# Optimization experiments

Hardware: AMD Instinct MI355X
Metric: run time of the kernel (lower is better)

The kernel has to match this reference:

```python
import jax, jax.numpy as jnp
import numpy as np

B, C, L, H, K, STRIDE = 8, 512, 2048, 8, 3, 1
D = C // H                       # head dim = 64
LQ = (L - K) // STRIDE + 1       # 'valid' conv output length = 2046
LN_EPS = 1e-5


def setup_inputs() -> dict:
    key = jax.random.key(0)
    ks = jax.random.split(key, 6)
    std = np.sqrt(2.0 / (C + C // H))  # init: sqrt(2 / sum(param.shape[:2]))
    inp = {
        "input": jax.random.normal(ks[0], (B, C, L), dtype=jnp.float32),
        "init_weight": jax.random.normal(ks[1], (B, C, LQ), dtype=jnp.float32),
        "q_w": jax.random.normal(ks[2], (C, C // H, K), dtype=jnp.float32) * std,
        "k_w": jax.random.normal(ks[3], (C, C // H, K), dtype=jnp.float32) * std,
        "v_w": jax.random.normal(ks[4], (C, C // H, K), dtype=jnp.float32) * std,
        "gamma": jnp.ones((C,), dtype=jnp.float32),
        "beta": jnp.zeros((C,), dtype=jnp.float32),
        # causal-style additive mask (1 above diagonal -> attention -= 1e9*mask)
        "mask": jnp.triu(jnp.ones((LQ, LQ), dtype=jnp.float32), k=1),
    }
    return inp


def _gconv(x, w):
    # x: [B, C, L], w: [C_out, C_in/groups, K] (torch OIH layout)
    return jax.lax.conv_general_dilated(
        x, w, window_strides=(STRIDE,), padding="VALID",
        dimension_numbers=("NCH", "OIH", "NCH"), feature_group_count=H)


def reference(input, init_weight, q_w, k_w, v_w, gamma, beta, mask):
    # grouped-conv QKV projections: [B, C, LQ]
    q = _gconv(input, q_w).reshape(B, H, D, LQ)
    k = _gconv(input, k_w).reshape(B, H, D, LQ)
    v = _gconv(input, v_w).reshape(B, H, D, LQ)

    # scores: q^T k per head; NOTE: faithful scale is 1/sqrt(multihead_num)
    att = jnp.einsum("bhdq,bhdk->bhqk", q, k)
    att = att / jnp.sqrt(jnp.asarray(H, att.dtype))
    att = att - 1e9 * mask  # broadcast [LQ, LQ] over [B, H, LQ, LQ]
    att = jax.nn.softmax(att, axis=-1)
    # dropout with p=0.0 is the identity (drop_rate=0.0)

    o = jnp.einsum("bhqk,bhdk->bhqd", att, v)          # [B, H, LQ, D]
    o = o.transpose(0, 2, 1, 3).reshape(B, LQ, C)       # merge heads (head-major channels)

    feat = o + init_weight.transpose(0, 2, 1)           # residual, [B, LQ, C]
    mu = jnp.mean(feat, axis=-1, keepdims=True)
    var = jnp.var(feat, axis=-1, keepdims=True)
    feat = (feat - mu) / jnp.sqrt(var + LN_EPS) * gamma + beta
    return feat  # [B, LQ, C]
```

## Files before the change

### kernel.cpp

```cpp
#include <hip/hip_runtime.h>

#define LQN 2046
#define LL  2048
#define CC  512
#define DD  64

typedef float  f32x4 __attribute__((ext_vector_type(4)));
typedef float  f32x2 __attribute__((ext_vector_type(2)));
typedef __bf16 b16x8 __attribute__((ext_vector_type(8)));
typedef unsigned int u32x4 __attribute__((ext_vector_type(4)));
typedef unsigned int u32x2 __attribute__((ext_vector_type(2)));

static __device__ __forceinline__ unsigned short f2bf(float f) {
  union { float f; unsigned u; } v; v.f = f;
  return (unsigned short)((v.u + 0x7fffu + ((v.u >> 16) & 1u)) >> 16);
}

static __device__ __forceinline__ unsigned cvtpk(float lo, float hi) {
  unsigned r;
  asm("v_cvt_pk_bf16_f32 %0, %1, %2" : "=v"(r) : "v"(lo), "v"(hi));
  return r;
}

static __device__ __forceinline__ f32x4 mfma16(b16x8 a, b16x8 b, f32x4 c) {
  return __builtin_amdgcn_mfma_f32_16x16x32_bf16(a, b, c, 0, 0, 0);
}

static __device__ __forceinline__ void glds16(const unsigned short* g, unsigned short* l) {
  __builtin_amdgcn_global_load_lds(
      (const __attribute__((address_space(1))) unsigned int*)(g),
      (__attribute__((address_space(3))) unsigned int*)(l),
      16, 0, 0);
}

__global__ __launch_bounds__(256) void conv_qkv_kernel(
    const float* __restrict__ in, const float* __restrict__ qw,
    const float* __restrict__ kw, const float* __restrict__ vw,
    unsigned short* __restrict__ qo, unsigned short* __restrict__ ko,
    unsigned short* __restrict__ vo)
{
  __shared__ __align__(16) unsigned short inT[130 * 72];
  __shared__ __align__(16) unsigned short buf[128 * 72];

  const int tile = blockIdx.x, g = blockIdx.y, b = blockIdx.z;
  const int t0 = tile * 128;
  const int tid = threadIdx.x;
  const int lane = tid & 63;
  const int wv = tid >> 6;
  const int r0 = lane & 15, qh = lane >> 4;

  {
    const int ci = tid & 63, ch = tid >> 6;
    const float* src = in + ((size_t)(b * CC + g * 64 + ci)) * LL;
    #pragma unroll
    for (int i = 0; i < 8; ++i) {
      int t = ch * 32 + i * 4;
      f32x4 d = *(const f32x4*)(src + t0 + t);
      inT[(t + 0) * 72 + ci] = f2bf(d.x);
      inT[(t + 1) * 72 + ci] = f2bf(d.y);
      inT[(t + 2) * 72 + ci] = f2bf(d.z);
      inT[(t + 3) * 72 + ci] = f2bf(d.w);
    }
    if (ch == 0) {
      #pragma unroll
      for (int e = 0; e < 2; ++e) {
        int t = 128 + e;
        int tg = t0 + t; if (tg > LL - 1) tg = LL - 1;
        inT[t * 72 + ci] = f2bf(src[tg]);
      }
    }
  }
  __syncthreads();

  const float* wptr[3] = {qw, kw, vw};
  const f32x4 zero4 = {0.f, 0.f, 0.f, 0.f};

  for (int p = 0; p < 3; ++p) {
    b16x8 aW[6];
    {
      const float* wb = wptr[p] + (size_t)(g * 64 + wv * 16 + r0) * 192;
      #pragma unroll
      for (int kc = 0; kc < 6; ++kc) {
        const int ktap = kc >> 1;
        const int cib = (kc & 1) * 32 + qh * 8;
        union { b16x8 v; unsigned short u[8]; } fr;
        #pragma unroll
        for (int j = 0; j < 8; ++j)
          fr.u[j] = f2bf(wb[(cib + j) * 3 + ktap]);
        aW[kc] = fr.v;
      }
    }
    f32x4 acc[8];
    #pragma unroll
    for (int nt = 0; nt < 8; ++nt) acc[nt] = zero4;
    #pragma unroll
    for (int kc = 0; kc < 6; ++kc) {
      const int radd = kc >> 1;
      const int colh = (kc & 1) * 32 + qh * 8;
      #pragma unroll
      for (int nt = 0; nt < 8; ++nt) {
        const int trow = nt * 16 + r0 + radd;
        b16x8 bI = *(const b16x8*)&inT[trow * 72 + colh];
        acc[nt] = mfma16(aW[kc], bI, acc[nt]);
      }
    }
    __syncthreads();
    if (p < 2) {
      const float qscl = (p == 0) ? 0.51006979f : 1.0f;
      #pragma unroll
      for (int nt = 0; nt < 8; ++nt) {
        const int t = nt * 16 + r0;
        #pragma unroll
        for (int r = 0; r < 4; ++r)
          buf[t * 72 + wv * 16 + qh * 4 + r] = f2bf(acc[nt][r] * qscl);
      }
      __syncthreads();
      unsigned short* dst = (p == 0 ? qo : ko) +
          ((size_t)(b * 8 + g) * LQN + t0) * DD;
      #pragma unroll
      for (int it = 0; it < 4; ++it) {
        const int id = it * 256 + tid;
        const int t = id >> 3, c8 = id & 7;
        if (t0 + t < LQN)
          *(u32x4*)(dst + t * DD + c8 * 8) = *(const u32x4*)&buf[t * 72 + c8 * 8];
      }
    } else {
      #pragma unroll
      for (int nt = 0; nt < 8; ++nt) {
        const int t = nt * 16 + r0;
        #pragma unroll
        for (int r = 0; r < 4; ++r)
          buf[(wv * 16 + qh * 4 + r) * 136 + t] = f2bf(acc[nt][r]);
      }
      __syncthreads();
      unsigned short* dst = vo + ((size_t)(b * CC + g * 64)) * LL + t0;
      #pragma unroll
      for (int it = 0; it < 4; ++it) {
        const int id = it * 256 + tid;
        const int row = id >> 4, c16 = id & 15;
        *(u32x4*)(dst + (size_t)row * LL + c16 * 8) =
            *(const u32x4*)&buf[row * 136 + c16 * 8];
      }
    }
    __syncthreads();
  }
}

static __device__ __forceinline__ void attn_tile(
    const unsigned short* __restrict__ Kl, const unsigned short* __restrict__ Vl,
    unsigned short* __restrict__ Pl,
    bool diag, int wv, int r0, int qh,
    b16x8 aQ0, b16x8 aQ1,
    f32x4 (&o)[4], float& mrun, float& lrun)
{
  f32x4 s[4];
  __builtin_amdgcn_s_setprio(1);
  #pragma unroll
  for (int nt = 0; nt < 4; ++nt) {
    const int krow = nt * 16 + r0;
    const unsigned short* kr = Kl + krow * 64;
    const int sw = krow & 7;
    b16x8 k0 = *(const b16x8*)(kr + ((qh ^ sw) * 8));
    b16x8 k1 = *(const b16x8*)(kr + (((4 + qh) ^ sw) * 8));
    f32x4 acc = {0.f, 0.f, 0.f, 0.f};
    acc = mfma16(k0, aQ0, acc);
    s[nt] = mfma16(k1, aQ1, acc);
  }
  __builtin_amdgcn_s_setprio(0);
  if (diag) {
    const int rowl = wv * 16 + r0;
    #pragma unroll
    for (int nt = 0; nt < 4; ++nt) {
      #pragma unroll
      for (int rr = 0; rr < 4; ++rr)
        if (nt * 16 + qh * 4 + rr > rowl) s[nt][rr] = -1e30f;
    }
  }
  f32x4 m01, m23;
  #pragma unroll
  for (int rr = 0; rr < 4; ++rr) {
    m01[rr] = fmaxf(s[0][rr], s[1][rr]);
    m23[rr] = fmaxf(s[2][rr], s[3][rr]);
  }
  #pragma unroll
  for (int rr = 0; rr < 4; ++rr) m01[rr] = fmaxf(m01[rr], m23[rr]);
  float mt = fmaxf(fmaxf(m01[0], m01[1]), fmaxf(m01[2], m01[3]));
  mt = fmaxf(mt, __shfl_xor(mt, 16));
  mt = fmaxf(mt, __shfl_xor(mt, 32));
  const float mn = fmaxf(mrun, mt);
  const float corr = __builtin_amdgcn_exp2f(mrun - mn);
  mrun = mn;
  #pragma unroll
  for (int nt = 0; nt < 4; ++nt)
    #pragma unroll
    for (int rr = 0; rr < 4; ++rr)
      s[nt][rr] = __builtin_amdgcn_exp2f(s[nt][rr] - mn);
  f32x4 t01, t23;
  #pragma unroll
  for (int rr = 0; rr < 4; ++rr) {
    t01[rr] = s[0][rr] + s[1][rr];
    t23[rr] = s[2][rr] + s[3][rr];
  }
  #pragma unroll
  for (int rr = 0; rr < 4; ++rr) t01[rr] += t23[rr];
  float sum = (t01[0] + t01[1]) + (t01[2] + t01[3]);
  sum += __shfl_xor(sum, 16);
  sum += __shfl_xor(sum, 32);
  lrun = lrun * corr + sum;
  const int xr = r0 & 7;
  unsigned short* pw = Pl + r0 * 64 + (qh & 1) * 4;
  #pragma unroll
  for (int nt = 0; nt < 4; ++nt) {
    u32x2 w;
    w.x = cvtpk(s[nt][0], s[nt][1]);
    w.y = cvtpk(s[nt][2], s[nt][3]);
    *(u32x2*)(pw + (((nt * 2 + (qh >> 1)) ^ xr) * 8)) = w;
  }
  #pragma unroll
  for (int rr = 0; rr < 4; ++rr) {
    const float cq = __shfl(corr, qh * 4 + rr);
    o[0][rr] *= cq; o[1][rr] *= cq; o[2][rr] *= cq; o[3][rr] *= cq;
  }
  __builtin_amdgcn_s_setprio(1);
  #pragma unroll
  for (int kc = 0; kc < 2; ++kc) {
    b16x8 aP = *(const b16x8*)(Pl + r0 * 64 + (((kc * 4 + qh) ^ xr) * 8));
    #pragma unroll
    for (int dt = 0; dt < 4; ++dt) {
      const int vrow = dt * 16 + r0;
      b16x8 bv = *(const b16x8*)(Vl + vrow * 64 + (((kc * 4 + qh) ^ (vrow & 7)) * 8));
      o[dt] = mfma16(aP, bv, o[dt]);
    }
  }
  __builtin_amdgcn_s_setprio(0);
}

static __device__ __forceinline__ void issue_tile(
    const unsigned short*& kSrc, const unsigned short*& vSrc,
    unsigned short* kDst, unsigned short* vDst)
{
  glds16(kSrc,          kDst);
  glds16(kSrc + 8 * DD, kDst + 512);
  glds16(vSrc,          vDst);
  glds16(vSrc + 8 * LL, vDst + 512);
  kSrc += 64 * DD;
  vSrc += 64;
}

static __device__ __forceinline__ void attn_epilogue(
    unsigned short* smem, const float* __restrict__ initw,
    float* __restrict__ out, int b, int h, int qt,
    int tid, int wv, int r0, int qh,
    f32x4 (&o)[4], float lrun)
{
  __syncthreads();
  float* initL = (float*)smem;
  const int cc = tid >> 2, qgrp = (tid & 3) * 16;
  const float* src = initw + (size_t)(b * CC + h * 64 + cc) * LQN;
  #pragma unroll
  for (int u = 0; u < 8; ++u) {
    int col = qt * 64 + qgrp + u * 2;
    if (col > LQN - 2) col = LQN - 2;
    f32x2 d = *(const f32x2*)(src + col);
    initL[cc * 65 + qgrp + u * 2]     = d.x;
    initL[cc * 65 + qgrp + u * 2 + 1] = d.y;
  }
  __syncthreads();
  #pragma unroll
  for (int r = 0; r < 4; ++r) {
    const float lq = __shfl(lrun, qh * 4 + r);
    const int ql = wv * 16 + qh * 4 + r;
    const int qgl = qt * 64 + ql;
    if (qgl >= LQN) continue;
    const float invl = 1.0f / lq;
    float* dst = out + ((size_t)(b * LQN + qgl)) * CC + h * 64;
    #pragma unroll
    for (int dt = 0; dt < 4; ++dt)
      dst[dt * 16 + r0] = o[dt][r] * invl + initL[(dt * 16 + r0) * 65 + ql];
  }
}

__global__ __launch_bounds__(256) void attn_kernel(
    const unsigned short* __restrict__ qg, const unsigned short* __restrict__ kg,
    const unsigned short* __restrict__ vg, const float* __restrict__ initw,
    float* __restrict__ out)
{
  __shared__ __align__(16) unsigned short KV[2][8192];
  __shared__ __align__(16) unsigned short Pb[4][1024];

  const int pi = blockIdx.x;
  const int hi = 31 - pi, lo = pi;
  const int bh = blockIdx.y;
  const int b = bh >> 3, h = bh & 7;
  const int tid = threadIdx.x, lane = tid & 63, wv = tid >> 6;
  const int r0 = lane & 15, qh = lane >> 4;

  const size_t kqbase = (size_t)bh * LQN * DD;
  const size_t vbase  = ((size_t)(b * CC + h * 64)) * LL;

  const int l8 = lane >> 3, c8s = lane & 7;
  const int csw = c8s ^ l8;
  const unsigned short* kSrc = kg + kqbase + (size_t)(wv * 16 + l8) * DD + csw * 8;
  const unsigned short* vSrc = vg + vbase  + (size_t)(wv * 16 + l8) * LL + csw * 8;

  b16x8 aQ0h, aQ1h, aQ0l, aQ1l;
  {
    int qrow = hi * 64 + wv * 16 + r0; if (qrow > LQN - 1) qrow = LQN - 1;
    const unsigned short* qp = qg + kqbase + (size_t)qrow * DD;
    aQ0h = *(const b16x8*)(qp + qh * 8);
    aQ1h = *(const b16x8*)(qp + 32 + qh * 8);
    qrow = lo * 64 + wv * 16 + r0;
    qp = qg + kqbase + (size_t)qrow * DD;
    aQ0l = *(const b16x8*)(qp + qh * 8);
    aQ1l = *(const b16x8*)(qp + 32 + qh * 8);
  }

  const f32x4 zero4 = {0.f, 0.f, 0.f, 0.f};
  f32x4 oh[4], ol[4];
  float mh = -1e30f, ml = -1e30f, lh = 0.f, llr = 0.f;
  #pragma unroll
  for (int dt = 0; dt < 4; ++dt) { oh[dt] = zero4; ol[dt] = zero4; }

  int bi = 0;
  issue_tile(kSrc, vSrc, &KV[0][wv * 1024], &KV[0][4096 + wv * 1024]);
  for (int kt = 0; kt <= hi; ++kt) {
    __syncthreads();
    if (kt < hi)
      issue_tile(kSrc, vSrc, &KV[bi ^ 1][wv * 1024], &KV[bi ^ 1][4096 + wv * 1024]);
    attn_tile(&KV[bi][0], &KV[bi][4096], Pb[wv], kt == hi, wv, r0, qh,
              aQ0h, aQ1h, oh, mh, lh);
    if (kt <= lo)
      attn_tile(&KV[bi][0], &KV[bi][4096], Pb[wv], kt == lo, wv, r0, qh,
                aQ0l, aQ1l, ol, ml, llr);
    bi ^= 1;
  }

  attn_epilogue(&KV[0][0], initw, out, b, h, hi, tid, wv, r0, qh, oh, lh);
  attn_epilogue(&KV[0][0], initw, out, b, h, lo, tid, wv, r0, qh, ol, llr);
}

__global__ __launch_bounds__(256) void ln_kernel(
    const float* __restrict__ gamma, const float* __restrict__ beta,
    float* __restrict__ out)
{
  const int row = blockIdx.x * 4 + ((int)threadIdx.x >> 6);
  const int lane = threadIdx.x & 63;
  if (row >= 8 * LQN) return;
  float* p = out + (size_t)row * CC;
  f32x4 x0 = *(const f32x4*)(p + lane * 8);
  f32x4 x1 = *(const f32x4*)(p + lane * 8 + 4);
  float s  = x0.x + x0.y + x0.z + x0.w + x1.x + x1.y + x1.z + x1.w;
  float sq = x0.x*x0.x + x0.y*x0.y + x0.z*x0.z + x0.w*x0.w
           + x1.x*x1.x + x1.y*x1.y + x1.z*x1.z + x1.w*x1.w;
  #pragma unroll
  for (int mm = 1; mm <= 32; mm <<= 1) {
    s  += __shfl_xor(s, mm);
    sq += __shfl_xor(sq, mm);
  }
  const float mu = s * (1.f / 512.f);
  const float var = sq * (1.f / 512.f) - mu * mu;
  const float rstd = rsqrtf(var + 1e-5f);
  f32x4 g0 = *(const f32x4*)(gamma + lane * 8);
  f32x4 g1 = *(const f32x4*)(gamma + lane * 8 + 4);
  f32x4 b0 = *(const f32x4*)(beta + lane * 8);
  f32x4 b1 = *(const f32x4*)(beta + lane * 8 + 4);
  x0 = (x0 - mu) * rstd * g0 + b0;
  x1 = (x1 - mu) * rstd * g1 + b1;
  *(f32x4*)(p + lane * 8)     = x0;
  *(f32x4*)(p + lane * 8 + 4) = x1;
}

extern "C" void kernel_launch(void* const* d_in, const int* in_sizes, int n_in,
                              void* d_out, int out_size, void* d_ws, size_t ws_size,
                              hipStream_t stream)
{
  const float* input = (const float*)d_in[0];
  const float* initw = (const float*)d_in[1];
  const float* qw    = (const float*)d_in[2];
  const float* kw    = (const float*)d_in[3];
  const float* vw    = (const float*)d_in[4];
  const float* gamma = (const float*)d_in[5];
  const float* beta  = (const float*)d_in[6];
  float* outp = (float*)d_out;

  unsigned short* q = (unsigned short*)d_ws;
  unsigned short* k = q + (16u * 1024u * 1024u / 2u);
  unsigned short* v = q + (32u * 1024u * 1024u / 2u);

  hipLaunchKernelGGL(conv_qkv_kernel, dim3(16, 8, 8), dim3(256), 0, stream,
                     input, qw, kw, vw, q, k, v);
  hipLaunchKernelGGL(attn_kernel, dim3(16, 64), dim3(256), 0, stream,
                     q, k, v, initw, outp);
  hipLaunchKernelGGL(ln_kernel, dim3(4092), dim3(256), 0, stream,
                     gamma, beta, outp);
}
```

Measured before the change: 151.5 us.

## Software-pipeline attention loop so PV of previous tile overlaps QK^T of current

Splits the attention tile into QK^T, softmax/pack and PV stages. The PV product for tile kt-1 now runs in iteration kt, after the QK^T of tile kt, with P held in registers. V loads are shifted one tile behind K loads so each V tile arrives a stage later. The goal is to hide the softmax dependency latency and the LDS traffic between the MFMA phases. The cost is a more complex control flow, with extra prologue and epilogue PV calls and more live registers, which may lower occupancy.

```diff
diff --git a/kernel.cpp b/kernel.cpp
--- a/kernel.cpp
+++ b/kernel.cpp
@@ -146,20 +146,16 @@
   }
 }
 
-static __device__ __forceinline__ void attn_tile(
-    const unsigned short* __restrict__ Kl, const unsigned short* __restrict__ Vl,
-    unsigned short* __restrict__ Pl,
-    bool diag, int wv, int r0, int qh,
-    b16x8 aQ0, b16x8 aQ1,
-    f32x4 (&o)[4], float& mrun, float& lrun)
-{
-  f32x4 s[4];
+
+static __device__ __forceinline__ void qkt16(
+    const unsigned short* __restrict__ Kl, bool diag, int wv, int r0, int qh,
+    b16x8 aQ0, b16x8 aQ1, f32x4 (&s)[4])
+{
+  const int sw = r0 & 7;
   __builtin_amdgcn_s_setprio(1);
   #pragma unroll
   for (int nt = 0; nt < 4; ++nt) {
-    const int krow = nt * 16 + r0;
-    const unsigned short* kr = Kl + krow * 64;
-    const int sw = krow & 7;
+    const unsigned short* kr = Kl + (nt * 16 + r0) * 64;
     b16x8 k0 = *(const b16x8*)(kr + ((qh ^ sw) * 8));
     b16x8 k1 = *(const b16x8*)(kr + (((4 + qh) ^ sw) * 8));
     f32x4 acc = {0.f, 0.f, 0.f, 0.f};
@@ -170,12 +166,35 @@
   if (diag) {
     const int rowl = wv * 16 + r0;
     #pragma unroll
-    for (int nt = 0; nt < 4; ++nt) {
+    for (int nt = 0; nt < 4; ++nt)
       #pragma unroll
       for (int rr = 0; rr < 4; ++rr)
         if (nt * 16 + qh * 4 + rr > rowl) s[nt][rr] = -1e30f;
-    }
-  }
+  }
+}
+
+static __device__ __forceinline__ void pv16(
+    const unsigned short* __restrict__ Vl, int r0, int qh,
+    b16x8 aP0, b16x8 aP1, f32x4 (&o)[4])
+{
+  const int sw = r0 & 7;
+  __builtin_amdgcn_s_setprio(1);
+  #pragma unroll
+  for (int dt = 0; dt < 4; ++dt) {
+    const unsigned short* vr = Vl + (dt * 16 + r0) * 64;
+    b16x8 bv0 = *(const b16x8*)(vr + ((qh ^ sw) * 8));
+    b16x8 bv1 = *(const b16x8*)(vr + (((4 + qh) ^ sw) * 8));
+    o[dt] = mfma16(aP0, bv0, o[dt]);
+    o[dt] = mfma16(aP1, bv1, o[dt]);
+  }
+  __builtin_amdgcn_s_setprio(0);
+}
+
+static __device__ __forceinline__ void softmax_pack(
+    f32x4 (&s)[4], f32x4 (&o)[4], float& mrun, float& lrun,
+    unsigned short* __restrict__ Pl, int r0, int qh,
+    b16x8& aP0, b16x8& aP1)
+{
   f32x4 m01, m23;
   #pragma unroll
   for (int rr = 0; rr < 4; ++rr) {
@@ -221,30 +240,8 @@
     const float cq = __shfl(corr, qh * 4 + rr);
     o[0][rr] *= cq; o[1][rr] *= cq; o[2][rr] *= cq; o[3][rr] *= cq;
   }
-  __builtin_amdgcn_s_setprio(1);
-  #pragma unroll
-  for (int kc = 0; kc < 2; ++kc) {
-    b16x8 aP = *(const b16x8*)(Pl + r0 * 64 + (((kc * 4 + qh) ^ xr) * 8));
-    #pragma unroll
-    for (int dt = 0; dt < 4; ++dt) {
-      const int vrow = dt * 16 + r0;
-      b16x8 bv = *(const b16x8*)(Vl + vrow * 64 + (((kc * 4 + qh) ^ (vrow & 7)) * 8));
-      o[dt] = mfma16(aP, bv, o[dt]);
-    }
-  }
-  __builtin_amdgcn_s_setprio(0);
-}
-
-static __device__ __forceinline__ void issue_tile(
-    const unsigned short*& kSrc, const unsigned short*& vSrc,
-    unsigned short* kDst, unsigned short* vDst)
-{
-  glds16(kSrc,          kDst);
-  glds16(kSrc + 8 * DD, kDst + 512);
-  glds16(vSrc,          vDst);
-  glds16(vSrc + 8 * LL, vDst + 512);
-  kSrc += 64 * DD;
-  vSrc += 64;
+  aP0 = *(const b16x8*)(Pl + r0 * 64 + ((qh ^ xr) * 8));
+  aP1 = *(const b16x8*)(Pl + r0 * 64 + (((4 + qh) ^ xr) * 8));
 }
 
 static __device__ __forceinline__ void attn_epilogue(
@@ -320,20 +317,40 @@
   float mh = -1e30f, ml = -1e30f, lh = 0.f, llr = 0.f;
   #pragma unroll
   for (int dt = 0; dt < 4; ++dt) { oh[dt] = zero4; ol[dt] = zero4; }
+  b16x8 aPh0, aPh1, aPl0, aPl1;
 
   int bi = 0;
-  issue_tile(kSrc, vSrc, &KV[0][wv * 1024], &KV[0][4096 + wv * 1024]);
+  glds16(kSrc,          &KV[0][wv * 1024]);
+  glds16(kSrc + 8 * DD, &KV[0][wv * 1024 + 512]);
+  kSrc += 64 * DD;
+
   for (int kt = 0; kt <= hi; ++kt) {
     __syncthreads();
-    if (kt < hi)
-      issue_tile(kSrc, vSrc, &KV[bi ^ 1][wv * 1024], &KV[bi ^ 1][4096 + wv * 1024]);
-    attn_tile(&KV[bi][0], &KV[bi][4096], Pb[wv], kt == hi, wv, r0, qh,
-              aQ0h, aQ1h, oh, mh, lh);
-    if (kt <= lo)
-      attn_tile(&KV[bi][0], &KV[bi][4096], Pb[wv], kt == lo, wv, r0, qh,
-                aQ0l, aQ1l, ol, ml, llr);
+    if (kt < hi) {
+      glds16(kSrc,          &KV[bi ^ 1][wv * 1024]);
+      glds16(kSrc + 8 * DD, &KV[bi ^ 1][wv * 1024 + 512]);
+      kSrc += 64 * DD;
+    }
+    glds16(vSrc,          &KV[bi ^ 1][4096 + wv * 1024]);
+    glds16(vSrc + 8 * LL, &KV[bi ^ 1][4096 + wv * 1024 + 512]);
+    vSrc += 64;
+
+    f32x4 sh[4];
+    qkt16(&KV[bi][0], kt == hi, wv, r0, qh, aQ0h, aQ1h, sh);
+    if (kt) pv16(&KV[bi][4096], r0, qh, aPh0, aPh1, oh);
+    softmax_pack(sh, oh, mh, lh, Pb[wv], r0, qh, aPh0, aPh1);
+    if (kt <= lo) {
+      f32x4 sl[4];
+      qkt16(&KV[bi][0], kt == lo, wv, r0, qh, aQ0l, aQ1l, sl);
+      if (kt) pv16(&KV[bi][4096], r0, qh, aPl0, aPl1, ol);
+      softmax_pack(sl, ol, ml, llr, Pb[wv], r0, qh, aPl0, aPl1);
+    } else if (kt == lo + 1) {
+      pv16(&KV[bi][4096], r0, qh, aPl0, aPl1, ol);
+    }
     bi ^= 1;
   }
+  __syncthreads();
+  pv16(&KV[bi][4096], r0, qh, aPh0, aPh1, oh);
 
   attn_epilogue(&KV[0][0], initw, out, b, h, hi, tid, wv, r0, qh, oh, lh);
   attn_epilogue(&KV[0][0], initw, out, b, h, lo, tid, wv, r0, qh, ol, llr);
```

Measured after the change: 154.3 us. No clear change (+1.9%).
